# Performance work log

Measured on AMD Instinct MI355X. Metric: run time of the kernel, lower is better.

## Reference

```python
import jax, jax.numpy as jnp
import numpy as np
import math

B, N, C, H = 4, 4096, 1024, 4
D = C // H            # per-head channel dim = 256
KV_SIZE = 1024        # config.KV_sizec, used as the score scale
EPS = 1e-5            # InstanceNorm2d default eps


def setup_inputs() -> dict:
    key = jax.random.key(0)
    ks = jax.random.split(key, 9)
    f = lambda k, shape: jax.random.normal(k, shape, dtype=jnp.float32) * 0.05
    return {
        'S':   f(ks[0], (B, N, C)),
        'SKV': f(ks[1], (B, N, C)),
        'T':   f(ks[2], (B, N, C)),
        'TKV': f(ks[3], (B, N, C)),
        'Wq':  f(ks[4], (H, D, D)),   # per-head torch Linear weights [out,in]
        'Wk':  f(ks[5], (H, D, D)),
        'Wv':  f(ks[6], (H, D, D)),
        'Wout':  f(ks[7], (C, C)),
        'Woutd': f(ks[8], (C, C)),
    }


def _heads(x, W):
    # x: [B,N,C] split into H chunks of D along channels; per-head Linear (no bias).
    xh = x.reshape(B, N, H, D)
    return jnp.einsum('bnhd,hed->bhne', xh, W)  # [B,H,N,D]


def _inorm(s):
    # InstanceNorm2d (affine=False): normalize over the last two dims per (batch, head).
    m = jnp.mean(s, axis=(-2, -1), keepdims=True)
    v = jnp.var(s, axis=(-2, -1), keepdims=True)
    return (s - m) * jax.lax.rsqrt(v + EPS)


def _attend(Q, K, V, Wout):
    # Channel attention: scores [B,H,D,D], sequence dim contracted.
    scores = jnp.einsum('bhni,bhnj->bhij', Q, K) / math.sqrt(KV_SIZE)
    probs = jax.nn.softmax(_inorm(scores), axis=-1)
    ctx = jnp.einsum('bhij,bhnj->bhin', probs, V)          # [B,H,D,N]
    # permute(0,3,2,1) -> [B,N,D,H], then view merges (D,H) with head fastest.
    ctx = jnp.transpose(ctx, (0, 3, 2, 1)).reshape(B, N, C)
    return jnp.einsum('bnc,oc->bno', ctx, Wout)


def reference(S, SKV, T, TKV, Wq, Wk, Wv, Wout, Woutd):
    Q  = _heads(S,   Wq); K  = _heads(SKV, Wk); V  = _heads(SKV, Wv)
    Qd = _heads(T,   Wq); Kd = _heads(TKV, Wk); Vd = _heads(TKV, Wv)
    S2T   = _attend(Q,  Kd, Vd, Wout)   # cross: S queries, T keys/values
    T2S   = _attend(Qd, K,  V,  Woutd)  # cross: T queries, S keys/values
    S_out = _attend(Q,  K,  V,  Wout)   # self on S
    T_out = _attend(Qd, Kd, Vd, Woutd)  # self on T
    return (S_out, T2S, S2T, T_out)
```

## Files before the change

### kernel.cpp

```cpp
#include <hip/hip_runtime.h>
#include <hip/hip_bf16.h>
#include <cstdint>

using bf16 = __hip_bfloat16;
typedef __attribute__((ext_vector_type(8))) short bf16x8v;
typedef __attribute__((ext_vector_type(4))) float f32x4v;

__device__ __forceinline__ void gload_lds16(const void* g, void* l) {
  __builtin_amdgcn_global_load_lds(
      (const __attribute__((address_space(1))) void*)g,
      (__attribute__((address_space(3))) void*)l, 16, 0, 0);
}

__device__ __forceinline__ unsigned short f2bu(float x) {
  union { __hip_bfloat16 h; unsigned short u; } cv;
  cv.h = __float2bfloat16(x);
  return cv.u;
}

__device__ __forceinline__ bf16x8v cvt8(const f32x4v lo, const f32x4v hi) {
  bf16x8v t;
  t[0] = (short)f2bu(lo[0]); t[1] = (short)f2bu(lo[1]);
  t[2] = (short)f2bu(lo[2]); t[3] = (short)f2bu(lo[3]);
  t[4] = (short)f2bu(hi[0]); t[5] = (short)f2bu(hi[1]);
  t[6] = (short)f2bu(hi[2]); t[7] = (short)f2bu(hi[3]);
  return t;
}

struct GemmP {
  const void* A; const void* B; const void* A2; const void* B2; void* C;
  int K, lda, ldb, ldc, tilesN, swz;
  int d0, d1, d2;
  long long sA0, sA1, sA2, sA3;
  long long sB0, sB1, sB2, sB3;
  long long sC0, sC1, sC2, sC3;
  long long zA, zB, zC;
  float scale;
};

template<int OUT_F32, int AF32, int BF32>
__global__ __launch_bounds__(256, 4)
void gemm_bt(GemmP p)
{
  constexpr int EA = AF32 ? 4 : 2;
  constexpr int EB = BF32 ? 4 : 2;
  constexpr int ABYTES = 128 * 64 * EA;
  constexpr int BBYTES = 128 * 64 * EB;
  constexpr int SEGA = ABYTES / 4096;
  constexpr int SEGB = BBYTES / 4096;
  __shared__ __attribute__((aligned(1024))) char smem[ABYTES + BBYTES];
  const int tid  = threadIdx.x;
  const int lane = tid & 63;
  const int wid  = tid >> 6;

  int bx = blockIdx.x;
  if (p.swz) {
    const int nx = gridDim.x;
    const int q = nx >> 3, r = nx & 7;
    const int xcd = bx & 7, loc = bx >> 3;
    bx = (xcd < r ? xcd * (q + 1) : r * (q + 1) + (xcd - r) * q) + loc;
  }
  const int tn = bx % p.tilesN;
  const int tm = bx / p.tilesN;
  int idx = blockIdx.y;
  const int i0 = idx % p.d0; idx /= p.d0;
  const int i1 = idx % p.d1; idx /= p.d1;
  const int i2 = idx % p.d2;
  const int i3 = idx / p.d2;

  const char* Abase = (const char*)((p.A2 && i2) ? p.A2 : p.A);
  const char* Bbase = (const char*)((p.B2 && i2) ? p.B2 : p.B);
  const long long offA = (long long)i0*p.sA0 + (long long)i1*p.sA1 +
                         (long long)i2*p.sA2 + (long long)i3*p.sA3 +
                         (long long)blockIdx.z*p.zA;
  const long long offB = (long long)i0*p.sB0 + (long long)i1*p.sB1 +
                         (long long)i2*p.sB2 + (long long)i3*p.sB3 +
                         (long long)blockIdx.z*p.zB;
  const char* Am = Abase + offA * EA;
  const char* Bm = Bbase + offB * EB;
  const int bm = tm * 128, bn = tn * 128;

  const char* asrc[SEGA]; int aseg[SEGA];
  #pragma unroll
  for (int r = 0; r < SEGA; ++r) {
    const int oseg = (wid * SEGA + r) * 1024;
    const int o = oseg + lane * 16;
    int row, srcoff;
    if constexpr (AF32) { row = o >> 8; const int s = (o >> 4) & 15; srcoff = (s ^ (row & 15)) * 4; }
    else               { row = o >> 7; const int s = (o >> 4) & 7;  srcoff = (s ^ (row & 7)) * 8;  }
    aseg[r] = oseg;
    asrc[r] = Am + ((long long)(bm + row) * p.lda + srcoff) * EA;
  }
  const char* bsrc[SEGB]; int bseg[SEGB];
  #pragma unroll
  for (int r = 0; r < SEGB; ++r) {
    const int oseg = (wid * SEGB + r) * 1024;
    const int o = oseg + lane * 16;
    int row, srcoff;
    if constexpr (BF32) { row = o >> 8; const int s = (o >> 4) & 15; srcoff = (s ^ (row & 15)) * 4; }
    else               { row = o >> 7; const int s = (o >> 4) & 7;  srcoff = (s ^ (row & 7)) * 8;  }
    bseg[r] = oseg;
    bsrc[r] = Bm + ((long long)(bn + row) * p.ldb + srcoff) * EB;
  }

  f32x4v acc[4][4];
  #pragma unroll
  for (int i = 0; i < 4; ++i)
    #pragma unroll
    for (int j = 0; j < 4; ++j) acc[i][j] = (f32x4v){0.f, 0.f, 0.f, 0.f};

  const int wr = wid >> 1, wc = wid & 1;
  const int fr_a = wr * 64 + (lane & 15);
  const int fr_b = wc * 64 + (lane & 15);
  const int fch  = lane >> 4;

  const int nK = p.K / 64;
  for (int kt = 0; kt < nK; ++kt) {
    #pragma unroll
    for (int r = 0; r < SEGA; ++r) { gload_lds16(asrc[r], smem + aseg[r]); asrc[r] += 64 * EA; }
    #pragma unroll
    for (int r = 0; r < SEGB; ++r) { gload_lds16(bsrc[r], smem + ABYTES + bseg[r]); bsrc[r] += 64 * EB; }
    __syncthreads();
    #pragma unroll
    for (int kk = 0; kk < 2; ++kk) {
      bf16x8v a[4], b[4];
      #pragma unroll
      for (int mi = 0; mi < 4; ++mi) {
        const int row = fr_a + mi * 16;
        if constexpr (AF32) {
          const int c2 = (fch + kk * 4) * 2;
          const f32x4v lo = *(const f32x4v*)(smem + row * 256 + ((c2 ^ (row & 15)) << 4));
          const f32x4v hi = *(const f32x4v*)(smem + row * 256 + (((c2 + 1) ^ (row & 15)) << 4));
          a[mi] = cvt8(lo, hi);
        } else {
          a[mi] = *(const bf16x8v*)(smem + row * 128 + (((fch + kk * 4) ^ (row & 7)) << 4));
        }
      }
      #pragma unroll
      for (int ni = 0; ni < 4; ++ni) {
        const int row = fr_b + ni * 16;
        if constexpr (BF32) {
          const int c2 = (fch + kk * 4) * 2;
          const f32x4v lo = *(const f32x4v*)(smem + ABYTES + row * 256 + ((c2 ^ (row & 15)) << 4));
          const f32x4v hi = *(const f32x4v*)(smem + ABYTES + row * 256 + (((c2 + 1) ^ (row & 15)) << 4));
          b[ni] = cvt8(lo, hi);
        } else {
          b[ni] = *(const bf16x8v*)(smem + ABYTES + row * 128 + (((fch + kk * 4) ^ (row & 7)) << 4));
        }
      }
      #pragma unroll
      for (int mi = 0; mi < 4; ++mi)
        #pragma unroll
        for (int ni = 0; ni < 4; ++ni)
          acc[mi][ni] = __builtin_amdgcn_mfma_f32_16x16x32_bf16(a[mi], b[ni], acc[mi][ni], 0, 0, 0);
    }
    __syncthreads();
  }

  const long long coff = (long long)i0*p.sC0 + (long long)i1*p.sC1 +
                         (long long)i2*p.sC2 + (long long)i3*p.sC3 +
                         (long long)blockIdx.z*p.zC;
  const int col0 = bn + wc * 64 + (lane & 15);
  const int row0 = bm + wr * 64 + ((lane >> 4) << 2);
  if (OUT_F32) {
    float* Cp = (float*)p.C + coff;
    #pragma unroll
    for (int mi = 0; mi < 4; ++mi)
      #pragma unroll
      for (int ni = 0; ni < 4; ++ni)
        #pragma unroll
        for (int j = 0; j < 4; ++j)
          Cp[(size_t)(row0 + mi*16 + j) * p.ldc + (col0 + ni*16)] = acc[mi][ni][j] * p.scale;
  } else {
    bf16* Cp = (bf16*)p.C + coff;
    #pragma unroll
    for (int mi = 0; mi < 4; ++mi)
      #pragma unroll
      for (int ni = 0; ni < 4; ++ni)
        #pragma unroll
        for (int j = 0; j < 4; ++j)
          Cp[(size_t)(row0 + mi*16 + j) * p.ldc + (col0 + ni*16)] =
              __float2bfloat16(acc[mi][ni][j] * p.scale);
  }
}

__global__ void cvt3_f32_bf16(const float* __restrict__ a0, const float* __restrict__ a1,
                              const float* __restrict__ a2,
                              unsigned short* __restrict__ out, long long ostride, int n4) {
  const int i = blockIdx.x * 256 + threadIdx.x;
  if (i >= n4) return;
  const float* src = (blockIdx.y == 0) ? a0 : (blockIdx.y == 1) ? a1 : a2;
  const float4 v = ((const float4*)src)[i];
  ushort4 o;
  o.x = f2bu(v.x); o.y = f2bu(v.y); o.z = f2bu(v.z); o.w = f2bu(v.w);
  ((ushort4*)(out + (size_t)blockIdx.y * ostride))[i] = o;
}

__global__ void wpre_kernel(const float* __restrict__ Wout, const float* __restrict__ Woutd,
                            bf16* __restrict__ Wpre) {
  const int w = blockIdx.y;
  const int flat = blockIdx.x * 256 + threadIdx.x;
  const float* Wsrc = w ? Woutd : Wout;
  const int o  = flat >> 10;
  const int c2 = flat & 1023;
  const int h  = c2 >> 8;
  const int i  = c2 & 255;
  Wpre[(size_t)w * 1048576 + flat] = __float2bfloat16(Wsrc[o * 1024 + i * 4 + h]);
}

__global__ __launch_bounds__(256)
void inorm_softmax_t4(const float* __restrict__ sp, bf16* __restrict__ pr) {
  const int m = blockIdx.x >> 2, q = blockIdx.x & 3;
  const size_t PS = 4194304;
  const float* s = sp + (size_t)m * 65536;
  const int tid = threadIdx.x, lane = tid & 63, w = tid >> 6;

  float sum = 0.f, sq = 0.f;
  for (int i = tid; i < 16384; i += 256) {
    const float4 a = ((const float4*)s)[i];
    const float4 b = ((const float4*)(s + PS))[i];
    const float4 c = ((const float4*)(s + 2 * PS))[i];
    const float4 d = ((const float4*)(s + 3 * PS))[i];
    const float x0 = (a.x + b.x) + (c.x + d.x);
    const float x1 = (a.y + b.y) + (c.y + d.y);
    const float x2 = (a.z + b.z) + (c.z + d.z);
    const float x3 = (a.w + b.w) + (c.w + d.w);
    sum += (x0 + x1) + (x2 + x3);
    sq  += (x0 * x0 + x1 * x1) + (x2 * x2 + x3 * x3);
  }
  #pragma unroll
  for (int o = 32; o; o >>= 1) { sum += __shfl_xor(sum, o); sq += __shfl_xor(sq, o); }
  __shared__ float red[8];
  __shared__ float seb[256];
  if (lane == 0) { red[w] = sum; red[4 + w] = sq; }
  __syncthreads();
  sum = red[0] + red[1] + red[2] + red[3];
  sq  = red[4] + red[5] + red[6] + red[7];
  const float mean = sum * (1.f / 65536.f);
  const float var  = sq * (1.f / 65536.f) - mean * mean;
  const float inv  = rsqrtf(var + 1e-5f);

  const int col = q * 64 + (tid & 63);
  const int j0  = (tid >> 6) * 64;
  const float* cb = s + col;
  float se = 0.f;
  for (int j = j0; j < j0 + 64; ++j) {
    const size_t o = (size_t)j * 256;
    const float v = (cb[o] + cb[PS + o]) + (cb[2 * PS + o] + cb[3 * PS + o]);
    se += __expf((v - mean) * inv);
  }
  seb[tid] = se;
  __syncthreads();
  const int c64 = tid & 63;
  const float rvs = 1.f / (((seb[c64] + seb[c64 + 64]) + (seb[c64 + 128] + seb[c64 + 192])));
  bf16* pc = pr + (size_t)m * 65536 + col;
  for (int j = j0; j < j0 + 64; ++j) {
    const size_t o = (size_t)j * 256;
    const float v = (cb[o] + cb[PS + o]) + (cb[2 * PS + o] + cb[3 * PS + o]);
    pc[o] = __float2bfloat16(__expf((v - mean) * inv) * rvs);
  }
}

extern "C" void kernel_launch(void* const* d_in, const int* in_sizes, int n_in,
                              void* d_out, int out_size, void* d_ws, size_t ws_size,
                              hipStream_t stream)
{
  const float* S     = (const float*)d_in[0];
  const float* SKV   = (const float*)d_in[1];
  const float* T     = (const float*)d_in[2];
  const float* TKV   = (const float*)d_in[3];
  const float* Wq    = (const float*)d_in[4];
  const float* Wk    = (const float*)d_in[5];
  const float* Wv    = (const float*)d_in[6];
  const float* Wout  = (const float*)d_in[7];
  const float* Woutd = (const float*)d_in[8];
  float* out = (float*)d_out;

  const int Hd = 4, Dd = 256;
  const long long NC  = 4096ll * 1024;
  const long long BNC = 4 * NC;
  const long long HDN = 1048576;

  char* ws = (char*)d_ws;
  size_t off = 0;
  auto alloc = [&](size_t bytes) -> void* {
    void* pp = ws + off; off += (bytes + 255) & ~(size_t)255; return pp;
  };
  bf16*  Wqb    = (bf16*)alloc((size_t)Hd * Dd * Dd * 2);
  bf16*  Wkb    = (bf16*)alloc((size_t)Hd * Dd * Dd * 2);
  bf16*  Wvb    = (bf16*)alloc((size_t)Hd * Dd * Dd * 2);
  bf16*  Wpre   = (bf16*)alloc(2ull * 1024 * 1024 * 2);
  bf16*  QT     = (bf16*)alloc(2 * BNC * 2);
  bf16*  KT     = (bf16*)alloc(2 * BNC * 2);
  bf16*  Vc     = (bf16*)alloc(2 * BNC * 2);
  float* sparts = (float*)alloc(4ull * 4194304 * 4);
  bf16*  probsT = (bf16*)alloc(64ull * 65536 * 2);
  bf16*  Weff   = QT;
  if (ws_size < off) return;

  {
    const int w4 = (Hd * Dd * Dd) / 4;
    cvt3_f32_bf16<<<dim3((w4 + 255) / 256, 3), dim3(256), 0, stream>>>(
        Wq, Wk, Wv, (unsigned short*)Wqb, (long long)Hd * Dd * Dd, w4);
    wpre_kernel<<<dim3(4096, 2), dim3(256), 0, stream>>>(Wout, Woutd, Wpre);
  }

  GemmP g{};

  g.A = Wqb; g.B = S; g.A2 = nullptr; g.B2 = T; g.C = QT;
  g.K = 256; g.lda = 256; g.ldb = 1024; g.ldc = 4096; g.tilesN = 32; g.swz = 0;
  g.d0 = 4; g.d1 = 4; g.d2 = 2;
  g.sA0 = 65536; g.sA1 = 0;  g.sA2 = 0;   g.sA3 = 0;
  g.sB0 = 256;   g.sB1 = NC; g.sB2 = 0;   g.sB3 = 0;
  g.sC0 = HDN;   g.sC1 = NC; g.sC2 = BNC; g.sC3 = 0;
  g.zA = 0; g.zB = 0; g.zC = 0;
  g.scale = 1.f;
  gemm_bt<0, 0, 1><<<dim3(2 * 32, 32), dim3(256), 0, stream>>>(g);

  g.A = Wkb; g.B = SKV; g.B2 = TKV; g.C = KT;
  gemm_bt<0, 0, 1><<<dim3(2 * 32, 32), dim3(256), 0, stream>>>(g);

  g.A = SKV; g.A2 = TKV; g.B = Wvb; g.B2 = nullptr; g.C = Vc;
  g.K = 256; g.lda = 1024; g.ldb = 256; g.ldc = 1024; g.tilesN = 2; g.swz = 0;
  g.sA0 = 256;   g.sA1 = NC; g.sA2 = 0; g.sA3 = 0;
  g.sB0 = 65536; g.sB1 = 0;  g.sB2 = 0; g.sB3 = 0;
  g.sC0 = 256;   g.sC1 = NC; g.sC2 = BNC; g.sC3 = 0;
  gemm_bt<0, 1, 0><<<dim3(32 * 2, 32), dim3(256), 0, stream>>>(g);

  g.A = KT; g.B = QT; g.A2 = nullptr; g.B2 = nullptr; g.C = sparts;
  g.K = 1024; g.lda = 4096; g.ldb = 4096; g.ldc = 256; g.tilesN = 2; g.swz = 0;
  g.d0 = 4; g.d1 = 4; g.d2 = 2;
  g.sA0 = HDN;   g.sA1 = NC;     g.sA2 = BNC;     g.sA3 = 0;
  g.sB0 = HDN;   g.sB1 = NC;     g.sB2 = 0;       g.sB3 = BNC;
  g.sC0 = 65536; g.sC1 = 262144; g.sC2 = 1048576; g.sC3 = 2097152;
  g.zA = 1024; g.zB = 1024; g.zC = 4194304;
  g.scale = 0.03125f;
  gemm_bt<1, 0, 0><<<dim3(2 * 2, 64, 4), dim3(256), 0, stream>>>(g);

  inorm_softmax_t4<<<dim3(256), dim3(256), 0, stream>>>(sparts, probsT);

  g.A = Wpre; g.B = probsT; g.C = Weff;
  g.K = 256; g.lda = 1024; g.ldb = 256; g.ldc = 1024; g.tilesN = 2; g.swz = 0;
  g.d0 = 4; g.d1 = 4; g.d2 = 2;
  g.sA0 = 256;   g.sA1 = 0;       g.sA2 = 0;       g.sA3 = 1048576;
  g.sB0 = 65536; g.sB1 = 262144;  g.sB2 = 1048576; g.sB3 = 2097152;
  g.sC0 = 256;   g.sC1 = 1048576; g.sC2 = 4194304; g.sC3 = 8388608;
  g.zA = 0; g.zB = 0; g.zC = 0;
  g.scale = 1.f;
  gemm_bt<0, 0, 0><<<dim3(8 * 2, 64), dim3(256), 0, stream>>>(g);

  g.A = Vc; g.B = Weff; g.C = out;
  g.K = 1024; g.lda = 1024; g.ldb = 1024; g.ldc = 1024; g.tilesN = 8; g.swz = 1;
  g.d0 = 4; g.d1 = 2; g.d2 = 2;
  g.sA0 = NC;      g.sA1 = BNC;     g.sA2 = 0;       g.sA3 = 0;
  g.sB0 = 1048576; g.sB1 = 4194304; g.sB2 = 8388608; g.sB3 = 0;
  g.sC0 = NC;      g.sC1 = 2 * BNC; g.sC2 = BNC;     g.sC3 = 0;
  g.scale = 1.f;
  gemm_bt<1, 0, 0><<<dim3(32 * 8, 16), dim3(256), 0, stream>>>(g);

  (void)in_sizes; (void)n_in; (void)out_size;
}
```

Before: 473.1 us.

## Fuse K and V projections into one kernel and split inorm-softmax stats pass

Replaces the separate K and V projection GEMMs with a single kernel that loads each fp32 SKV/TKV tile once into LDS and computes both K^T and V outputs with MFMA. This avoids reading the fp32 activations twice and removes one launch. It also splits the instance-norm/softmax kernel into a stats kernel that parallelizes the mean/variance reduction across 4 blocks per matrix, and a softmax kernel that keeps exponentials in registers instead of re-reading and recomputing them. The costs are higher register pressure (two accumulator sets, a 64-entry array) and one extra launch.

```diff
diff --git a/kernel.cpp b/kernel.cpp
--- a/kernel.cpp
+++ b/kernel.cpp
@@ -184,6 +184,115 @@
   }
 }
 
+struct KVP {
+  const float* X0; const float* X1;
+  const bf16* Wk; const bf16* Wv;
+  bf16* KT; bf16* Vc;
+};
+
+__global__ __launch_bounds__(256, 2)
+void kv_fused(KVP p)
+{
+  __shared__ __attribute__((aligned(1024))) char smem[65536];
+  const int tid = threadIdx.x, lane = tid & 63, wid = tid >> 6;
+  const int jt = blockIdx.x & 1, nt = blockIdx.x >> 1;
+  int idx = blockIdx.y;
+  const int h = idx & 3; idx >>= 2;
+  const int b = idx & 3; idx >>= 2;
+  const int vi = idx;
+  const float* X = (vi ? p.X1 : p.X0) + (size_t)b * 4194304 + (size_t)h * 256;
+  const bf16* Wk = p.Wk + (size_t)h * 65536;
+  const bf16* Wv = p.Wv + (size_t)h * 65536;
+  const int n0 = nt * 128, j0 = jt * 128;
+
+  const float* xsrc[8];
+  #pragma unroll
+  for (int r = 0; r < 8; ++r) {
+    const int o = (wid * 8 + r) * 1024 + lane * 16;
+    const int row = o >> 8, s = (o >> 4) & 15;
+    xsrc[r] = X + (size_t)(n0 + row) * 1024 + (s ^ (row & 15)) * 4;
+  }
+  const bf16 *wksrc[4], *wvsrc[4];
+  #pragma unroll
+  for (int r = 0; r < 4; ++r) {
+    const int o = (wid * 4 + r) * 1024 + lane * 16;
+    const int row = o >> 7, s = (o >> 4) & 7;
+    wksrc[r] = Wk + (size_t)(j0 + row) * 256 + (s ^ (row & 7)) * 8;
+    wvsrc[r] = Wv + (size_t)(j0 + row) * 256 + (s ^ (row & 7)) * 8;
+  }
+
+  f32x4v accK[4][4], accV[4][4];
+  #pragma unroll
+  for (int i = 0; i < 4; ++i)
+    #pragma unroll
+    for (int j = 0; j < 4; ++j) {
+      accK[i][j] = (f32x4v){0.f, 0.f, 0.f, 0.f};
+      accV[i][j] = (f32x4v){0.f, 0.f, 0.f, 0.f};
+    }
+
+  const int wr = wid >> 1, wc = wid & 1;
+  const int frW = wr * 64 + (lane & 15);
+  const int frX = wc * 64 + (lane & 15);
+  const int fch = lane >> 4;
+
+  for (int kt = 0; kt < 4; ++kt) {
+    #pragma unroll
+    for (int r = 0; r < 8; ++r) { gload_lds16(xsrc[r], smem + (wid * 8 + r) * 1024); xsrc[r] += 64; }
+    #pragma unroll
+    for (int r = 0; r < 4; ++r) {
+      gload_lds16(wksrc[r], smem + 32768 + (wid * 4 + r) * 1024); wksrc[r] += 64;
+      gload_lds16(wvsrc[r], smem + 49152 + (wid * 4 + r) * 1024); wvsrc[r] += 64;
+    }
+    __syncthreads();
+    #pragma unroll
+    for (int kk = 0; kk < 2; ++kk) {
+      bf16x8v wk[4], wv[4], x[4];
+      #pragma unroll
+      for (int mi = 0; mi < 4; ++mi) {
+        const int row = frW + mi * 16;
+        const int byo = row * 128 + (((fch + kk * 4) ^ (row & 7)) << 4);
+        wk[mi] = *(const bf16x8v*)(smem + 32768 + byo);
+        wv[mi] = *(const bf16x8v*)(smem + 49152 + byo);
+      }
+      #pragma unroll
+      for (int ni = 0; ni < 4; ++ni) {
+        const int row = frX + ni * 16;
+        const int c2 = (fch + kk * 4) * 2;
+        const f32x4v lo = *(const f32x4v*)(smem + row * 256 + ((c2 ^ (row & 15)) << 4));
+        const f32x4v hi = *(const f32x4v*)(smem + row * 256 + (((c2 + 1) ^ (row & 15)) << 4));
+        x[ni] = cvt8(lo, hi);
+      }
+      #pragma unroll
+      for (int mi = 0; mi < 4; ++mi)
+        #pragma unroll
+        for (int ni = 0; ni < 4; ++ni) {
+          accK[mi][ni] = __builtin_amdgcn_mfma_f32_16x16x32_bf16(wk[mi], x[ni], accK[mi][ni], 0, 0, 0);
+          accV[ni][mi] = __builtin_amdgcn_mfma_f32_16x16x32_bf16(x[ni], wv[mi], accV[ni][mi], 0, 0, 0);
+        }
+    }
+    __syncthreads();
+  }
+
+  const size_t kbase = (size_t)vi * 16777216 + (size_t)b * 4194304 + (size_t)h * 1048576;
+  const size_t vbase = (size_t)vi * 16777216 + (size_t)b * 4194304;
+  bf16* Kp = p.KT + kbase;
+  bf16* Vp = p.Vc + vbase;
+  const int rW = ((lane >> 4) << 2);
+  #pragma unroll
+  for (int mi = 0; mi < 4; ++mi)
+    #pragma unroll
+    for (int ni = 0; ni < 4; ++ni)
+      #pragma unroll
+      for (int j = 0; j < 4; ++j) {
+        const int jrow = j0 + wr * 64 + mi * 16 + rW + j;
+        const int ncol = n0 + wc * 64 + ni * 16 + (lane & 15);
+        Kp[(size_t)jrow * 4096 + ncol] = __float2bfloat16(accK[mi][ni][j]);
+        const int nrow = n0 + wc * 64 + ni * 16 + rW + j;
+        const int jcol = j0 + wr * 64 + mi * 16 + (lane & 15);
+        Vp[(size_t)nrow * 1024 + h * 256 + jcol] = __float2bfloat16(accV[ni][mi][j]);
+      }
+}
+
 __global__ void cvt3_f32_bf16(const float* __restrict__ a0, const float* __restrict__ a1,
                               const float* __restrict__ a2,
                               unsigned short* __restrict__ out, long long ostride, int n4) {
@@ -209,14 +318,14 @@
 }
 
 __global__ __launch_bounds__(256)
-void inorm_softmax_t4(const float* __restrict__ sp, bf16* __restrict__ pr) {
+void stats_quarter(const float* __restrict__ sp, float* __restrict__ st) {
   const int m = blockIdx.x >> 2, q = blockIdx.x & 3;
   const size_t PS = 4194304;
-  const float* s = sp + (size_t)m * 65536;
+  const float* s = sp + (size_t)m * 65536 + (size_t)q * 16384;
   const int tid = threadIdx.x, lane = tid & 63, w = tid >> 6;
 
   float sum = 0.f, sq = 0.f;
-  for (int i = tid; i < 16384; i += 256) {
+  for (int i = tid; i < 4096; i += 256) {
     const float4 a = ((const float4*)s)[i];
     const float4 b = ((const float4*)(s + PS))[i];
     const float4 c = ((const float4*)(s + 2 * PS))[i];
@@ -231,34 +340,48 @@
   #pragma unroll
   for (int o = 32; o; o >>= 1) { sum += __shfl_xor(sum, o); sq += __shfl_xor(sq, o); }
   __shared__ float red[8];
-  __shared__ float seb[256];
   if (lane == 0) { red[w] = sum; red[4 + w] = sq; }
   __syncthreads();
-  sum = red[0] + red[1] + red[2] + red[3];
-  sq  = red[4] + red[5] + red[6] + red[7];
+  if (tid == 0) {
+    st[blockIdx.x * 2]     = (red[0] + red[1]) + (red[2] + red[3]);
+    st[blockIdx.x * 2 + 1] = (red[4] + red[5]) + (red[6] + red[7]);
+  }
+}
+
+__global__ __launch_bounds__(256)
+void softmax_t(const float* __restrict__ sp, const float* __restrict__ st,
+               bf16* __restrict__ pr) {
+  const int m = blockIdx.x >> 2, iq = blockIdx.x & 3;
+  const size_t PS = 4194304;
+  const float sum = (st[m*8+0] + st[m*8+2]) + (st[m*8+4] + st[m*8+6]);
+  const float sq  = (st[m*8+1] + st[m*8+3]) + (st[m*8+5] + st[m*8+7]);
   const float mean = sum * (1.f / 65536.f);
   const float var  = sq * (1.f / 65536.f) - mean * mean;
   const float inv  = rsqrtf(var + 1e-5f);
 
-  const int col = q * 64 + (tid & 63);
-  const int j0  = (tid >> 6) * 64;
-  const float* cb = s + col;
+  const int tid = threadIdx.x;
+  const int i  = iq * 64 + (tid & 63);
+  const int jq = tid >> 6;
+  const float* cb = sp + (size_t)m * 65536 + i;
+
+  float e[64];
   float se = 0.f;
-  for (int j = j0; j < j0 + 64; ++j) {
-    const size_t o = (size_t)j * 256;
+  #pragma unroll
+  for (int jj = 0; jj < 64; ++jj) {
+    const size_t o = (size_t)(jq * 64 + jj) * 256;
     const float v = (cb[o] + cb[PS + o]) + (cb[2 * PS + o] + cb[3 * PS + o]);
-    se += __expf((v - mean) * inv);
-  }
+    e[jj] = __expf((v - mean) * inv);
+    se += e[jj];
+  }
+  __shared__ float seb[256];
   seb[tid] = se;
   __syncthreads();
-  const int c64 = tid & 63;
-  const float rvs = 1.f / (((seb[c64] + seb[c64 + 64]) + (seb[c64 + 128] + seb[c64 + 192])));
-  bf16* pc = pr + (size_t)m * 65536 + col;
-  for (int j = j0; j < j0 + 64; ++j) {
-    const size_t o = (size_t)j * 256;
-    const float v = (cb[o] + cb[PS + o]) + (cb[2 * PS + o] + cb[3 * PS + o]);
-    pc[o] = __float2bfloat16(__expf((v - mean) * inv) * rvs);
-  }
+  const int c = tid & 63;
+  const float rvs = 1.f / ((seb[c] + seb[c + 64]) + (seb[c + 128] + seb[c + 192]));
+  bf16* pc = pr + (size_t)m * 65536 + i;
+  #pragma unroll
+  for (int jj = 0; jj < 64; ++jj)
+    pc[(size_t)(jq * 64 + jj) * 256] = __float2bfloat16(e[jj] * rvs);
 }
 
 extern "C" void kernel_launch(void* const* d_in, const int* in_sizes, int n_in,
@@ -294,6 +417,7 @@
   bf16*  KT     = (bf16*)alloc(2 * BNC * 2);
   bf16*  Vc     = (bf16*)alloc(2 * BNC * 2);
   float* sparts = (float*)alloc(4ull * 4194304 * 4);
+  float* stats  = (float*)alloc(256ull * 2 * 4);
   bf16*  probsT = (bf16*)alloc(64ull * 65536 * 2);
   bf16*  Weff   = QT;
   if (ws_size < off) return;
@@ -317,15 +441,10 @@
   g.scale = 1.f;
   gemm_bt<0, 0, 1><<<dim3(2 * 32, 32), dim3(256), 0, stream>>>(g);
 
-  g.A = Wkb; g.B = SKV; g.B2 = TKV; g.C = KT;
-  gemm_bt<0, 0, 1><<<dim3(2 * 32, 32), dim3(256), 0, stream>>>(g);
-
-  g.A = SKV; g.A2 = TKV; g.B = Wvb; g.B2 = nullptr; g.C = Vc;
-  g.K = 256; g.lda = 1024; g.ldb = 256; g.ldc = 1024; g.tilesN = 2; g.swz = 0;
-  g.sA0 = 256;   g.sA1 = NC; g.sA2 = 0; g.sA3 = 0;
-  g.sB0 = 65536; g.sB1 = 0;  g.sB2 = 0; g.sB3 = 0;
-  g.sC0 = 256;   g.sC1 = NC; g.sC2 = BNC; g.sC3 = 0;
-  gemm_bt<0, 1, 0><<<dim3(32 * 2, 32), dim3(256), 0, stream>>>(g);
+  {
+    KVP kv{SKV, TKV, Wkb, Wvb, KT, Vc};
+    kv_fused<<<dim3(64, 32), dim3(256), 0, stream>>>(kv);
+  }
 
   g.A = KT; g.B = QT; g.A2 = nullptr; g.B2 = nullptr; g.C = sparts;
   g.K = 1024; g.lda = 4096; g.ldb = 4096; g.ldc = 256; g.tilesN = 2; g.swz = 0;
@@ -337,7 +456,8 @@
   g.scale = 0.03125f;
   gemm_bt<1, 0, 0><<<dim3(2 * 2, 64, 4), dim3(256), 0, stream>>>(g);
 
-  inorm_softmax_t4<<<dim3(256), dim3(256), 0, stream>>>(sparts, probsT);
+  stats_quarter<<<dim3(256), dim3(256), 0, stream>>>(sparts, stats);
+  softmax_t<<<dim3(256), dim3(256), 0, stream>>>(sparts, stats, probsT);
 
   g.A = Wpre; g.B = probsT; g.C = Weff;
   g.K = 256; g.lda = 1024; g.ldb = 256; g.ldc = 1024; g.tilesN = 2; g.swz = 0;
```

Measured after the change: 445.3 us. -5.9%, faster.
